# Optimization experiments

Hardware: AMD Instinct MI355X
Metric: run time of the kernel (lower is better)

## Reference

```python
import jax, jax.numpy as jnp
import numpy as np

B, T, D, A = 64, 2048, 512, 128

def setup_inputs() -> dict:
    key = jax.random.key(0)
    k_x, k_w1, k_b1, k_w2, k_b2 = jax.random.split(key, 5)
    s1 = 1.0 / np.sqrt(D)
    s2 = 1.0 / np.sqrt(A)
    return {
        "x": jax.random.normal(k_x, (B, T, D), dtype=jnp.float32),
        "W1": jax.random.uniform(k_w1, (D, A), minval=-s1, maxval=s1, dtype=jnp.float32),
        "b1": jax.random.uniform(k_b1, (A,), minval=-s1, maxval=s1, dtype=jnp.float32),
        "W2": jax.random.uniform(k_w2, (A, 1), minval=-s2, maxval=s2, dtype=jnp.float32),
        "b2": jax.random.uniform(k_b2, (1,), minval=-s2, maxval=s2, dtype=jnp.float32),
    }

def reference(x, W1, b1, W2, b2):
    # attention scores: [B, T, 1]
    h = jnp.tanh(jnp.einsum('btd,da->bta', x, W1) + b1)
    scores = jnp.einsum('bta,ao->bto', h, W2) + b2
    w = jax.nn.softmax(scores, axis=1)              # [B, T, 1]
    mu = jnp.sum(x * w, axis=1)                     # [B, D]
    var = jnp.sum((x - mu[:, None, :]) ** 2 * w, axis=1)
    std = jnp.sqrt(var + 1e-6)
    return jnp.concatenate([mu, std], axis=-1)      # [B, 2D]
```

## Files before the change

### kernel.cpp

```cpp
#include <hip/hip_runtime.h>
#include <hip/hip_bf16.h>
#include <math.h>

#define B_ 64
#define T_ 2048
#define D_ 512
#define A_ 128

typedef __bf16 bf16x8 __attribute__((ext_vector_type(8)));
typedef float  f32x4  __attribute__((ext_vector_type(4)));

__global__ __launch_bounds__(256) void prep_kernel(
    const float* __restrict__ W1, __hip_bfloat16* __restrict__ W1T)
{
    int idx = blockIdx.x * 256 + threadIdx.x;
    int k = idx >> 7;
    int n = idx & 127;
    W1T[n * D_ + k] = __float2bfloat16(W1[idx]);
}

__device__ inline bf16x8 cvt8(float4 a, float4 b) {
    bf16x8 r;
    r[0] = (__bf16)a.x; r[1] = (__bf16)a.y; r[2] = (__bf16)a.z; r[3] = (__bf16)a.w;
    r[4] = (__bf16)b.x; r[5] = (__bf16)b.y; r[6] = (__bf16)b.z; r[7] = (__bf16)b.w;
    return r;
}

__device__ inline float fast_tanh(float v) {
    v = fminf(fmaxf(v, -15.f), 15.f);
    float e = __expf(2.f * v);
    return (e - 1.f) / (e + 1.f);
}

__global__ __launch_bounds__(256) void scores_kernel(
    const float* __restrict__ x, const __hip_bfloat16* __restrict__ W1T_,
    const float* __restrict__ b1, const float* __restrict__ W2,
    const float* __restrict__ b2, float* __restrict__ scores)
{
    const __bf16* W1T = (const __bf16*)W1T_;
    const int tid  = threadIdx.x;
    const int wave = tid >> 6;
    const int lane = tid & 63;
    const int col  = lane & 15;
    const int kgrp = lane >> 4;

    const long tokbase = (long)blockIdx.x * 128 + wave * 32;

    f32x4 acc[8][2];
#pragma unroll
    for (int mt = 0; mt < 8; mt++) {
        acc[mt][0] = (f32x4){0.f, 0.f, 0.f, 0.f};
        acc[mt][1] = (f32x4){0.f, 0.f, 0.f, 0.f};
    }

    const float* xp0 = x + (tokbase + col) * D_;
    const float* xp1 = xp0 + 16 * D_;
    const __bf16* wp = W1T + (long)col * D_;

#pragma unroll 2
    for (int ks = 0; ks < 16; ks++) {
        const int klane = ks * 32 + kgrp * 8;
        float4 b0a = *(const float4*)(xp0 + klane);
        float4 b0b = *(const float4*)(xp0 + klane + 4);
        float4 b1a = *(const float4*)(xp1 + klane);
        float4 b1b = *(const float4*)(xp1 + klane + 4);
        bf16x8 bf0 = cvt8(b0a, b0b);
        bf16x8 bf1 = cvt8(b1a, b1b);
#pragma unroll
        for (int mt = 0; mt < 8; mt++) {
            bf16x8 af = *(const bf16x8*)(wp + (long)mt * 16 * D_ + klane);
            acc[mt][0] = __builtin_amdgcn_mfma_f32_16x16x32_bf16(af, bf0, acc[mt][0], 0, 0, 0);
            acc[mt][1] = __builtin_amdgcn_mfma_f32_16x16x32_bf16(af, bf1, acc[mt][1], 0, 0, 0);
        }
    }

    float p0 = 0.f, p1 = 0.f;
#pragma unroll
    for (int mt = 0; mt < 8; mt++) {
#pragma unroll
        for (int r = 0; r < 4; r++) {
            int n = mt * 16 + kgrp * 4 + r;
            float bb = b1[n];
            float ww = W2[n];
            p0 += fast_tanh(acc[mt][0][r] + bb) * ww;
            p1 += fast_tanh(acc[mt][1][r] + bb) * ww;
        }
    }
    p0 += __shfl_xor(p0, 16, 64);
    p0 += __shfl_xor(p0, 32, 64);
    p1 += __shfl_xor(p1, 16, 64);
    p1 += __shfl_xor(p1, 32, 64);
    if (lane < 16) {
        float bias = b2[0];
        scores[tokbase + col]      = p0 + bias;
        scores[tokbase + 16 + col] = p1 + bias;
    }
}

__global__ __launch_bounds__(256) void softmax_kernel(
    const float* __restrict__ scores, float* __restrict__ w)
{
    const int b = blockIdx.x;
    const int tid = threadIdx.x;
    const float* s = scores + (long)b * T_;

    float v[8];
    float mx = -1e30f;
#pragma unroll
    for (int j = 0; j < 8; j++) {
        v[j] = s[tid + j * 256];
        mx = fmaxf(mx, v[j]);
    }
#pragma unroll
    for (int off = 1; off < 64; off <<= 1)
        mx = fmaxf(mx, __shfl_xor(mx, off, 64));
    __shared__ float redm[4];
    if ((tid & 63) == 0) redm[tid >> 6] = mx;
    __syncthreads();
    mx = fmaxf(fmaxf(redm[0], redm[1]), fmaxf(redm[2], redm[3]));

    float sum = 0.f;
#pragma unroll
    for (int j = 0; j < 8; j++) {
        v[j] = __expf(v[j] - mx);
        sum += v[j];
    }
#pragma unroll
    for (int off = 1; off < 64; off <<= 1)
        sum += __shfl_xor(sum, off, 64);
    __shared__ float reds[4];
    if ((tid & 63) == 0) reds[tid >> 6] = sum;
    __syncthreads();
    sum = reds[0] + reds[1] + reds[2] + reds[3];
    const float inv = 1.0f / sum;
#pragma unroll
    for (int j = 0; j < 8; j++)
        w[(long)b * T_ + tid + j * 256] = v[j] * inv;
}

__global__ __launch_bounds__(256) void pool_partial_kernel(
    const float* __restrict__ x, const float* __restrict__ w,
    float* __restrict__ pmu, float* __restrict__ pm2)
{
    const int blk = blockIdx.x;
    const int b = blk >> 3;
    const int t0 = (blk & 7) * 256;
    const int tid = threadIdx.x;
    const int half = tid >> 7;
    const int dq = tid & 127;

    const float* wb = w + (long)b * T_ + t0;
    const float* xb = x + ((long)b * T_ + t0) * D_ + dq * 4;

    float4 mu = {0.f, 0.f, 0.f, 0.f};
    float4 m2 = {0.f, 0.f, 0.f, 0.f};

#pragma unroll 4
    for (int t = half; t < 256; t += 2) {
        float wt = wb[t];
        float4 xv = *(const float4*)(xb + (long)t * D_);
        mu.x = fmaf(wt, xv.x, mu.x);
        mu.y = fmaf(wt, xv.y, mu.y);
        mu.z = fmaf(wt, xv.z, mu.z);
        mu.w = fmaf(wt, xv.w, mu.w);
        m2.x = fmaf(wt * xv.x, xv.x, m2.x);
        m2.y = fmaf(wt * xv.y, xv.y, m2.y);
        m2.z = fmaf(wt * xv.z, xv.z, m2.z);
        m2.w = fmaf(wt * xv.w, xv.w, m2.w);
    }

    __shared__ float4 smu[256];
    __shared__ float4 sm2[256];
    smu[tid] = mu;
    sm2[tid] = m2;
    __syncthreads();

    if (tid < 128) {
        float4 a = smu[tid], c = smu[tid + 128];
        float4 e = sm2[tid], f = sm2[tid + 128];
        a.x += c.x; a.y += c.y; a.z += c.z; a.w += c.w;
        e.x += f.x; e.y += f.y; e.z += f.z; e.w += f.w;
        *(float4*)(pmu + (long)blk * D_ + dq * 4) = a;
        *(float4*)(pm2 + (long)blk * D_ + dq * 4) = e;
    }
}

__global__ __launch_bounds__(256) void pool_final_kernel(
    const float* __restrict__ pmu, const float* __restrict__ pm2,
    float* __restrict__ out)
{
    const int b = blockIdx.x;
    const int tid = threadIdx.x;
#pragma unroll
    for (int i = 0; i < 2; i++) {
        int d = tid + i * 256;
        float mu = 0.f, m2 = 0.f;
#pragma unroll
        for (int c = 0; c < 8; c++) {
            mu += pmu[((long)b * 8 + c) * D_ + d];
            m2 += pm2[((long)b * 8 + c) * D_ + d];
        }
        out[(long)b * (2 * D_) + d] = mu;
        out[(long)b * (2 * D_) + D_ + d] = sqrtf(fmaxf(m2 - mu * mu, 0.f) + 1e-6f);
    }
}

extern "C" void kernel_launch(void* const* d_in, const int* in_sizes, int n_in,
                              void* d_out, int out_size, void* d_ws, size_t ws_size,
                              hipStream_t stream) {
    const float* x  = (const float*)d_in[0];
    const float* W1 = (const float*)d_in[1];
    const float* b1 = (const float*)d_in[2];
    const float* W2 = (const float*)d_in[3];
    const float* b2 = (const float*)d_in[4];
    float* out = (float*)d_out;

    float* ws = (float*)d_ws;
    float* scores = ws;
    float* w      = ws + (long)B_ * T_;
    float* pmu    = ws + 2L * B_ * T_;
    float* pm2    = pmu + 512L * D_;
    __hip_bfloat16* W1T = (__hip_bfloat16*)(pm2 + 512L * D_);

    prep_kernel<<<256, 256, 0, stream>>>(W1, W1T);
    scores_kernel<<<(B_ * T_) / 128, 256, 0, stream>>>(x, W1T, b1, W2, b2, scores);
    softmax_kernel<<<B_, 256, 0, stream>>>(scores, w);
    pool_partial_kernel<<<B_ * 8, 256, 0, stream>>>(x, w, pmu, pm2);
    pool_final_kernel<<<B_, 256, 0, stream>>>(pmu, pm2, out);
}
```

Baseline: 428.7 us.

## Fuse scores, softmax and pooling into one single-pass kernel over x

```diff
diff --git a/kernel.cpp b/kernel.cpp
--- a/kernel.cpp
+++ b/kernel.cpp
@@ -6,6 +6,11 @@
 #define T_ 2048
 #define D_ 512
 #define A_ 128
+
+#define CHUNK  32
+#define NCHUNK 8
+#define SEG    (CHUNK*NCHUNK)
+#define NBLK   (B_*(T_/SEG))
 
 typedef __bf16 bf16x8 __attribute__((ext_vector_type(8)));
 typedef float  f32x4  __attribute__((ext_vector_type(4)));
@@ -32,177 +37,193 @@
     return (e - 1.f) / (e + 1.f);
 }
 
-__global__ __launch_bounds__(256) void scores_kernel(
+typedef __attribute__((address_space(1))) const void gas_t;
+typedef __attribute__((address_space(3))) void las_t;
+#define GLOAD_LDS16(g, l) \
+    __builtin_amdgcn_global_load_lds((gas_t*)(g), (las_t*)(l), 16, 0, 0)
+
+__global__ __launch_bounds__(256, 1) void fused_kernel(
     const float* __restrict__ x, const __hip_bfloat16* __restrict__ W1T_,
     const float* __restrict__ b1, const float* __restrict__ W2,
-    const float* __restrict__ b2, float* __restrict__ scores)
+    const float* __restrict__ b2,
+    float* __restrict__ pS, float* __restrict__ pmu, float* __restrict__ pm2)
 {
+    __shared__ __align__(16) float xs[2][CHUNK * D_];
+    __shared__ float parr[4][2][16];
+    __shared__ float uarr[CHUNK];
+
     const __bf16* W1T = (const __bf16*)W1T_;
     const int tid  = threadIdx.x;
-    const int wave = tid >> 6;
+    const int wv   = tid >> 6;
     const int lane = tid & 63;
     const int col  = lane & 15;
     const int kgrp = lane >> 4;
 
-    const long tokbase = (long)blockIdx.x * 128 + wave * 32;
-
-    f32x4 acc[8][2];
-#pragma unroll
-    for (int mt = 0; mt < 8; mt++) {
-        acc[mt][0] = (f32x4){0.f, 0.f, 0.f, 0.f};
-        acc[mt][1] = (f32x4){0.f, 0.f, 0.f, 0.f};
+    const int bk  = blockIdx.x;
+    const int b   = bk >> 3;
+    const int seg = bk & 7;
+    const float* xb = x + ((long)b * T_ + (long)seg * SEG) * D_;
+
+    bf16x8 af[2][16];
+#pragma unroll
+    for (int mtl = 0; mtl < 2; mtl++) {
+        const __bf16* wp = W1T + (long)((2*wv + mtl)*16 + col) * D_ + kgrp*8;
+#pragma unroll
+        for (int ks = 0; ks < 16; ks++)
+            af[mtl][ks] = *(const bf16x8*)(wp + ks*32);
     }
-
-    const float* xp0 = x + (tokbase + col) * D_;
-    const float* xp1 = xp0 + 16 * D_;
-    const __bf16* wp = W1T + (long)col * D_;
-
-#pragma unroll 2
-    for (int ks = 0; ks < 16; ks++) {
-        const int klane = ks * 32 + kgrp * 8;
-        float4 b0a = *(const float4*)(xp0 + klane);
-        float4 b0b = *(const float4*)(xp0 + klane + 4);
-        float4 b1a = *(const float4*)(xp1 + klane);
-        float4 b1b = *(const float4*)(xp1 + klane + 4);
-        bf16x8 bf0 = cvt8(b0a, b0b);
-        bf16x8 bf1 = cvt8(b1a, b1b);
-#pragma unroll
-        for (int mt = 0; mt < 8; mt++) {
-            bf16x8 af = *(const bf16x8*)(wp + (long)mt * 16 * D_ + klane);
-            acc[mt][0] = __builtin_amdgcn_mfma_f32_16x16x32_bf16(af, bf0, acc[mt][0], 0, 0, 0);
-            acc[mt][1] = __builtin_amdgcn_mfma_f32_16x16x32_bf16(af, bf1, acc[mt][1], 0, 0, 0);
-        }
+    float b1v[2][4], w2v[2][4];
+#pragma unroll
+    for (int mtl = 0; mtl < 2; mtl++)
+#pragma unroll
+        for (int r = 0; r < 4; r++) {
+            int n = (2*wv + mtl)*16 + kgrp*4 + r;
+            b1v[mtl][r] = b1[n];
+            w2v[mtl][r] = W2[n];
+        }
+    const float bias2 = b2[0];
+
+    float mu0 = 0.f, mu1 = 0.f, m20 = 0.f, m21 = 0.f, su = 0.f;
+
+    auto STAGE = [&](int bufi, int c) {
+        const float* src = xb + (long)c * (CHUNK * D_);
+        float* dstbase = &xs[bufi][0];
+#pragma unroll
+        for (int j = 0; j < 16; j++) {
+            int G = j*256 + tid;
+            int t = G >> 7;
+            int g = G & 127;
+            const float* gp = src + t*D_ + ((g ^ (t & 7)) << 2);
+            float* lp = dstbase + ((j*256 + wv*64) << 2);
+            GLOAD_LDS16(gp, lp);
+        }
+    };
+
+    STAGE(0, 0);
+    int cur = 0;
+
+    for (int c = 0; c < NCHUNK; c++) {
+        if (c + 1 < NCHUNK) {
+            STAGE(cur ^ 1, c + 1);
+            asm volatile("s_waitcnt vmcnt(16)" ::: "memory");
+        } else {
+            asm volatile("s_waitcnt vmcnt(0)" ::: "memory");
+        }
+        __builtin_amdgcn_s_barrier();
+        asm volatile("" ::: "memory");
+
+        const float* bufp = &xs[cur][0];
+
+        f32x4 acc[2][2];
+#pragma unroll
+        for (int mtl = 0; mtl < 2; mtl++)
+#pragma unroll
+            for (int tt = 0; tt < 2; tt++)
+                acc[mtl][tt] = (f32x4){0.f, 0.f, 0.f, 0.f};
+
+#pragma unroll
+        for (int ks = 0; ks < 16; ks++) {
+            bf16x8 bfr[2];
+#pragma unroll
+            for (int tt = 0; tt < 2; tt++) {
+                int t  = tt*16 + col;
+                int m  = t & 7;
+                int gb = ks*8 + kgrp*2;
+                float4 aa = *(const float4*)(bufp + (t << 9) + (((gb    ) ^ m) << 2));
+                float4 bb = *(const float4*)(bufp + (t << 9) + (((gb + 1) ^ m) << 2));
+                bfr[tt] = cvt8(aa, bb);
+            }
+#pragma unroll
+            for (int mtl = 0; mtl < 2; mtl++) {
+                acc[mtl][0] = __builtin_amdgcn_mfma_f32_16x16x32_bf16(af[mtl][ks], bfr[0], acc[mtl][0], 0, 0, 0);
+                acc[mtl][1] = __builtin_amdgcn_mfma_f32_16x16x32_bf16(af[mtl][ks], bfr[1], acc[mtl][1], 0, 0, 0);
+            }
+        }
+
+        float p0 = 0.f, p1 = 0.f;
+#pragma unroll
+        for (int mtl = 0; mtl < 2; mtl++)
+#pragma unroll
+            for (int r = 0; r < 4; r++) {
+                p0 += fast_tanh(acc[mtl][0][r] + b1v[mtl][r]) * w2v[mtl][r];
+                p1 += fast_tanh(acc[mtl][1][r] + b1v[mtl][r]) * w2v[mtl][r];
+            }
+        p0 += __shfl_xor(p0, 16, 64);
+        p0 += __shfl_xor(p0, 32, 64);
+        p1 += __shfl_xor(p1, 16, 64);
+        p1 += __shfl_xor(p1, 32, 64);
+        if (lane < 16) {
+            parr[wv][0][lane] = p0;
+            parr[wv][1][lane] = p1;
+        }
+        asm volatile("s_waitcnt lgkmcnt(0)" ::: "memory");
+        __builtin_amdgcn_s_barrier();
+        asm volatile("" ::: "memory");
+
+        if (tid < CHUNK) {
+            int tt = tid >> 4, cc = tid & 15;
+            float s = parr[0][tt][cc] + parr[1][tt][cc]
+                    + parr[2][tt][cc] + parr[3][tt][cc] + bias2;
+            uarr[tid] = __expf(s);
+        }
+        asm volatile("s_waitcnt lgkmcnt(0)" ::: "memory");
+        __builtin_amdgcn_s_barrier();
+        asm volatile("" ::: "memory");
+
+        const int gacc = tid >> 1;
+        const int fo   = (tid & 1) << 1;
+#pragma unroll
+        for (int t = 0; t < CHUNK; t++) {
+            float u = uarr[t];
+            const float* pp = bufp + (t << 9) + ((gacc ^ (t & 7)) << 2) + fo;
+            float2 xv = *(const float2*)pp;
+            mu0 = fmaf(u, xv.x, mu0);
+            mu1 = fmaf(u, xv.y, mu1);
+            m20 = fmaf(u * xv.x, xv.x, m20);
+            m21 = fmaf(u * xv.y, xv.y, m21);
+            su += u;
+        }
+        asm volatile("" ::: "memory");
+        __builtin_amdgcn_s_barrier();
+        asm volatile("" ::: "memory");
+
+        cur ^= 1;
     }
 
-    float p0 = 0.f, p1 = 0.f;
-#pragma unroll
-    for (int mt = 0; mt < 8; mt++) {
-#pragma unroll
-        for (int r = 0; r < 4; r++) {
-            int n = mt * 16 + kgrp * 4 + r;
-            float bb = b1[n];
-            float ww = W2[n];
-            p0 += fast_tanh(acc[mt][0][r] + bb) * ww;
-            p1 += fast_tanh(acc[mt][1][r] + bb) * ww;
-        }
+    const int d0 = tid * 2;
+    pmu[(long)bk * D_ + d0]     = mu0;
+    pmu[(long)bk * D_ + d0 + 1] = mu1;
+    pm2[(long)bk * D_ + d0]     = m20;
+    pm2[(long)bk * D_ + d0 + 1] = m21;
+    if (tid == 0) pS[bk] = su;
+}
+
+__global__ __launch_bounds__(256) void merge_kernel(
+    const float* __restrict__ pS, const float* __restrict__ pmu,
+    const float* __restrict__ pm2, float* __restrict__ out)
+{
+    const int b = blockIdx.x, tid = threadIdx.x;
+    float S = 0.f;
+#pragma unroll
+    for (int c = 0; c < 8; c++) S += pS[b*8 + c];
+    const float inv = 1.f / S;
+
+    const int d0 = tid * 2;
+    float mu0 = 0.f, mu1 = 0.f, m20 = 0.f, m21 = 0.f;
+#pragma unroll
+    for (int c = 0; c < 8; c++) {
+        const float* pb = pmu + (long)(b*8 + c) * D_ + d0;
+        const float* qb = pm2 + (long)(b*8 + c) * D_ + d0;
+        mu0 += pb[0]; mu1 += pb[1];
+        m20 += qb[0]; m21 += qb[1];
     }
-    p0 += __shfl_xor(p0, 16, 64);
-    p0 += __shfl_xor(p0, 32, 64);
-    p1 += __shfl_xor(p1, 16, 64);
-    p1 += __shfl_xor(p1, 32, 64);
-    if (lane < 16) {
-        float bias = b2[0];
-        scores[tokbase + col]      = p0 + bias;
-        scores[tokbase + 16 + col] = p1 + bias;
-    }
-}
-
-__global__ __launch_bounds__(256) void softmax_kernel(
-    const float* __restrict__ scores, float* __restrict__ w)
-{
-    const int b = blockIdx.x;
-    const int tid = threadIdx.x;
-    const float* s = scores + (long)b * T_;
-
-    float v[8];
-    float mx = -1e30f;
-#pragma unroll
-    for (int j = 0; j < 8; j++) {
-        v[j] = s[tid + j * 256];
-        mx = fmaxf(mx, v[j]);
-    }
-#pragma unroll
-    for (int off = 1; off < 64; off <<= 1)
-        mx = fmaxf(mx, __shfl_xor(mx, off, 64));
-    __shared__ float redm[4];
-    if ((tid & 63) == 0) redm[tid >> 6] = mx;
-    __syncthreads();
-    mx = fmaxf(fmaxf(redm[0], redm[1]), fmaxf(redm[2], redm[3]));
-
-    float sum = 0.f;
-#pragma unroll
-    for (int j = 0; j < 8; j++) {
-        v[j] = __expf(v[j] - mx);
-        sum += v[j];
-    }
-#pragma unroll
-    for (int off = 1; off < 64; off <<= 1)
-        sum += __shfl_xor(sum, off, 64);
-    __shared__ float reds[4];
-    if ((tid & 63) == 0) reds[tid >> 6] = sum;
-    __syncthreads();
-    sum = reds[0] + reds[1] + reds[2] + reds[3];
-    const float inv = 1.0f / sum;
-#pragma unroll
-    for (int j = 0; j < 8; j++)
-        w[(long)b * T_ + tid + j * 256] = v[j] * inv;
-}
-
-__global__ __launch_bounds__(256) void pool_partial_kernel(
-    const float* __restrict__ x, const float* __restrict__ w,
-    float* __restrict__ pmu, float* __restrict__ pm2)
-{
-    const int blk = blockIdx.x;
-    const int b = blk >> 3;
-    const int t0 = (blk & 7) * 256;
-    const int tid = threadIdx.x;
-    const int half = tid >> 7;
-    const int dq = tid & 127;
-
-    const float* wb = w + (long)b * T_ + t0;
-    const float* xb = x + ((long)b * T_ + t0) * D_ + dq * 4;
-
-    float4 mu = {0.f, 0.f, 0.f, 0.f};
-    float4 m2 = {0.f, 0.f, 0.f, 0.f};
-
-#pragma unroll 4
-    for (int t = half; t < 256; t += 2) {
-        float wt = wb[t];
-        float4 xv = *(const float4*)(xb + (long)t * D_);
-        mu.x = fmaf(wt, xv.x, mu.x);
-        mu.y = fmaf(wt, xv.y, mu.y);
-        mu.z = fmaf(wt, xv.z, mu.z);
-        mu.w = fmaf(wt, xv.w, mu.w);
-        m2.x = fmaf(wt * xv.x, xv.x, m2.x);
-        m2.y = fmaf(wt * xv.y, xv.y, m2.y);
-        m2.z = fmaf(wt * xv.z, xv.z, m2.z);
-        m2.w = fmaf(wt * xv.w, xv.w, m2.w);
-    }
-
-    __shared__ float4 smu[256];
-    __shared__ float4 sm2[256];
-    smu[tid] = mu;
-    sm2[tid] = m2;
-    __syncthreads();
-
-    if (tid < 128) {
-        float4 a = smu[tid], c = smu[tid + 128];
-        float4 e = sm2[tid], f = sm2[tid + 128];
-        a.x += c.x; a.y += c.y; a.z += c.z; a.w += c.w;
-        e.x += f.x; e.y += f.y; e.z += f.z; e.w += f.w;
-        *(float4*)(pmu + (long)blk * D_ + dq * 4) = a;
-        *(float4*)(pm2 + (long)blk * D_ + dq * 4) = e;
-    }
-}
-
-__global__ __launch_bounds__(256) void pool_final_kernel(
-    const float* __restrict__ pmu, const float* __restrict__ pm2,
-    float* __restrict__ out)
-{
-    const int b = blockIdx.x;
-    const int tid = threadIdx.x;
-#pragma unroll
-    for (int i = 0; i < 2; i++) {
-        int d = tid + i * 256;
-        float mu = 0.f, m2 = 0.f;
-#pragma unroll
-        for (int c = 0; c < 8; c++) {
-            mu += pmu[((long)b * 8 + c) * D_ + d];
-            m2 += pm2[((long)b * 8 + c) * D_ + d];
-        }
-        out[(long)b * (2 * D_) + d] = mu;
-        out[(long)b * (2 * D_) + D_ + d] = sqrtf(fmaxf(m2 - mu * mu, 0.f) + 1e-6f);
-    }
+    mu0 *= inv; mu1 *= inv; m20 *= inv; m21 *= inv;
+
+    float* ob = out + (long)b * (2 * D_);
+    ob[d0]     = mu0;
+    ob[d0 + 1] = mu1;
+    ob[D_ + d0]     = sqrtf(fmaxf(m20 - mu0 * mu0, 0.f) + 1e-6f);
+    ob[D_ + d0 + 1] = sqrtf(fmaxf(m21 - mu1 * mu1, 0.f) + 1e-6f);
 }
 
 extern "C" void kernel_launch(void* const* d_in, const int* in_sizes, int n_in,
@@ -216,15 +237,12 @@
     float* out = (float*)d_out;
 
     float* ws = (float*)d_ws;
-    float* scores = ws;
-    float* w      = ws + (long)B_ * T_;
-    float* pmu    = ws + 2L * B_ * T_;
-    float* pm2    = pmu + 512L * D_;
+    float* pS  = ws;
+    float* pmu = ws + 512;
+    float* pm2 = pmu + 512L * D_;
     __hip_bfloat16* W1T = (__hip_bfloat16*)(pm2 + 512L * D_);
 
     prep_kernel<<<256, 256, 0, stream>>>(W1, W1T);
-    scores_kernel<<<(B_ * T_) / 128, 256, 0, stream>>>(x, W1T, b1, W2, b2, scores);
-    softmax_kernel<<<B_, 256, 0, stream>>>(scores, w);
-    pool_partial_kernel<<<B_ * 8, 256, 0, stream>>>(x, w, pmu, pm2);
-    pool_final_kernel<<<B_, 256, 0, stream>>>(pmu, pm2, out);
-}
+    fused_kernel<<<NBLK, 256, 0, stream>>>(x, W1T, b1, W2, b2, pS, pmu, pm2);
+    merge_kernel<<<B_, 256, 0, stream>>>(pS, pmu, pm2, out);
+}
```

Result: faster. 387.8 us (-9.5%).
